# Kernel tuning notes

Hardware: AMD Instinct MI355X
Metric: run time of the kernel (lower is better)

The kernel has to match this reference:

```python
import jax, jax.numpy as jnp
import numpy as np


def gcn_conv(x, edge_index, W, b):
    # PyG GCNConv with normalize=True: add self-loops, symmetric D^-1/2 A D^-1/2,
    # transform then aggregate messages source->target, then add bias.
    N = x.shape[0]
    row, col = edge_index[0], edge_index[1]  # row: source, col: target
    loop = jnp.arange(N, dtype=edge_index.dtype)
    row = jnp.concatenate([row, loop])
    col = jnp.concatenate([col, loop])
    ones = jnp.ones(row.shape[0], dtype=x.dtype)
    deg = jax.ops.segment_sum(ones, col, num_segments=N)
    dinv = jnp.where(deg > 0, jax.lax.rsqrt(deg), 0.0)
    norm = dinv[row] * dinv[col]            # [E+N]
    h = x @ W                                # [N, d_out] transform first (cheaper aggregation)
    msgs = h[row] * norm[:, None]            # gather + scale
    out = jax.ops.segment_sum(msgs, col, num_segments=N)  # scatter-add to targets
    return out + b


def setup_inputs() -> dict:
    key = jax.random.key(0)
    k = jax.random.split(key, 6)
    N, D, H, C, E = 100000, 256, 32, 2, 3200000
    x = jax.random.normal(k[0], (N, D), dtype=jnp.float32)
    edge_index = jax.random.randint(k[1], (2, E), 0, N, dtype=jnp.int64)
    # glorot-style init for GCN weights
    W1 = jax.random.normal(k[2], (D, H), dtype=jnp.float32) * np.sqrt(2.0 / (D + H))
    b1 = jnp.zeros((H,), dtype=jnp.float32)
    W2 = jax.random.normal(k[3], (H, C), dtype=jnp.float32) * np.sqrt(2.0 / (H + C))
    b2 = jnp.zeros((C,), dtype=jnp.float32)
    return {"x": x, "edge_index": edge_index, "W1": W1, "b1": b1, "W2": W2, "b2": b2}


def reference(x, edge_index, W1, b1, W2, b2):
    # CRD: GCNConv -> relu -> dropout(p=0.5, eval mode -> identity)
    h = jax.nn.relu(gcn_conv(x, edge_index, W1, b1))
    # CLS: GCNConv -> log_softmax over classes
    logits = gcn_conv(h, edge_index, W2, b2)
    return jax.nn.log_softmax(logits, axis=1)
```

## Files before the change

### kernel.cpp

```cpp
#include <hip/hip_runtime.h>
#include <hip/hip_fp16.h>
#include <math.h>

#define DIV_UP(a,b) (((a)+(b)-1)/(b))

typedef _Float16 f16x8 __attribute__((ext_vector_type(8)));
typedef float    f32x4 __attribute__((ext_vector_type(4)));

#define SHIFT 9
#define TPB   (1 << SHIFT)
#define LMASK (TPB - 1)
#define CHUNK 4096

__global__ __launch_bounds__(256) void k_init(int* __restrict__ gcur, int cap,
                                              int* __restrict__ offsets, int N, int E) {
    const int t = threadIdx.x;
    gcur[t] = t * cap;
    if (t == 0) offsets[N] = E;
}

__global__ __launch_bounds__(256) void k_binA(const int* __restrict__ row,
                                              const int* __restrict__ col,
                                              int* __restrict__ gcur,
                                              unsigned* __restrict__ binned, int E) {
    __shared__ int hist[256], loff[256], gbase[256], lcur[256];
    __shared__ unsigned staged[CHUNK];
    __shared__ unsigned char binOf[CHUNK];
    const int t = threadIdx.x;
    const int base = blockIdx.x * CHUNK;
    const int n = min(CHUNK, E - base);

    hist[t] = 0;
    __syncthreads();

    unsigned pk[CHUNK / 256];
    int bn[CHUNK / 256];
#pragma unroll
    for (int k = 0; k < CHUNK / 256; ++k) {
        int i = base + t + k * 256;
        if (i < E) {
            int c = col[i], r = row[i];
            bn[k] = c >> SHIFT;
            pk[k] = ((unsigned)r << SHIFT) | (unsigned)(c & LMASK);
            atomicAdd(&hist[bn[k]], 1);
        } else bn[k] = -1;
    }
    __syncthreads();

    int v = hist[t];
    loff[t] = v;
    __syncthreads();
#pragma unroll
    for (int off = 1; off < 256; off <<= 1) {
        int y = (t >= off) ? loff[t - off] : 0;
        __syncthreads();
        loff[t] += y;
        __syncthreads();
    }
    int excl = loff[t] - v;
    gbase[t] = v ? atomicAdd(&gcur[t], v) : 0;
    lcur[t]  = excl;
    __syncthreads();
    loff[t] = excl;
    __syncthreads();

#pragma unroll
    for (int k = 0; k < CHUNK / 256; ++k) {
        if (bn[k] >= 0) {
            int p = atomicAdd(&lcur[bn[k]], 1);
            staged[p] = pk[k];
            binOf[p] = (unsigned char)bn[k];
        }
    }
    __syncthreads();

    for (int i = t; i < n; i += 256) {
        int b = binOf[i];
        binned[gbase[b] + (i - loff[b])] = staged[i];
    }
}

__global__ __launch_bounds__(256) void k_bscan2(const int* __restrict__ gcur, int cap,
                                                int* __restrict__ srcBase, int E) {
    __shared__ int sh[256];
    const int t = threadIdx.x;
    int cnt = gcur[t] - t * cap;
    sh[t] = cnt;
    __syncthreads();
#pragma unroll
    for (int off = 1; off < 256; off <<= 1) {
        int y = (t >= off) ? sh[t - off] : 0;
        __syncthreads();
        sh[t] += y;
        __syncthreads();
    }
    srcBase[t] = sh[t] - cnt;
    if (t == 255) srcBase[256] = E;
}

__global__ __launch_bounds__(512) void k_csr(const unsigned* __restrict__ binned,
                                             const int* __restrict__ gcur, int cap,
                                             const int* __restrict__ srcBase,
                                             int* __restrict__ offsets,
                                             float* __restrict__ dinv,
                                             int* __restrict__ srcs, int N) {
    __shared__ int h[TPB];
    __shared__ int cur[TPB];
    const int t = threadIdx.x, b = blockIdx.x;
    const int beg = b * cap, end = gcur[b];
    const int obase = srcBase[b];

    h[t] = 0;
    __syncthreads();
    for (int i = beg + t; i < end; i += 512)
        atomicAdd(&h[binned[i] & LMASK], 1);
    __syncthreads();

    int cnt = h[t];
#pragma unroll
    for (int off = 1; off < 512; off <<= 1) {
        int y = (t >= off) ? h[t - off] : 0;
        __syncthreads();
        h[t] += y;
        __syncthreads();
    }
    int excl = h[t] - cnt;
    int g = (b << SHIFT) + t;
    int pos0 = obase + excl;
    if (g < N) {
        offsets[g] = pos0;
        dinv[g] = rsqrtf((float)(1 + cnt));
    }
    cur[t] = pos0;
    __syncthreads();

    for (int i = beg + t; i < end; i += 512) {
        unsigned v = binned[i];
        int pos = atomicAdd(&cur[v & LMASK], 1);
        srcs[pos] = (int)(v >> SHIFT);
    }
}

__global__ __launch_bounds__(256) void k_gemm1(const float* __restrict__ x,
                                               const float* __restrict__ W,
                                               const float* __restrict__ dinv,
                                               __half* __restrict__ h1w, int N) {
    __shared__ float Wl[8192];
    const int t = threadIdx.x;

    const float4* W4 = (const float4*)W;
    float4* Wl4 = (float4*)Wl;
#pragma unroll
    for (int i = 0; i < 8; ++i) Wl4[t + 256 * i] = W4[t + 256 * i];
    __syncthreads();

    const int lane = t & 63;
    const int wv   = t >> 6;
    const int m    = lane & 15;
    const int q    = lane >> 4;

    f16x8 bf[8][2];
#pragma unroll
    for (int kc = 0; kc < 8; ++kc)
#pragma unroll
        for (int ct = 0; ct < 2; ++ct)
#pragma unroll
            for (int j = 0; j < 8; ++j)
                bf[kc][ct][j] = (_Float16)Wl[(kc * 32 + q * 8 + j) * 32 + ct * 16 + m];

    const int rowA   = blockIdx.x * 64 + wv * 16 + m;
    const int rclamp = min(rowA, N - 1);
    const float* xr  = x + (long long)rclamp * 256 + q * 8;

    f32x4 c0 = {0.f, 0.f, 0.f, 0.f}, c1 = {0.f, 0.f, 0.f, 0.f};
#pragma unroll
    for (int kc = 0; kc < 8; ++kc) {
        float4 v0 = *(const float4*)(xr + kc * 32);
        float4 v1 = *(const float4*)(xr + kc * 32 + 4);
        f16x8 a;
        a[0] = (_Float16)v0.x; a[1] = (_Float16)v0.y;
        a[2] = (_Float16)v0.z; a[3] = (_Float16)v0.w;
        a[4] = (_Float16)v1.x; a[5] = (_Float16)v1.y;
        a[6] = (_Float16)v1.z; a[7] = (_Float16)v1.w;
        c0 = __builtin_amdgcn_mfma_f32_16x16x32_f16(a, bf[kc][0], c0, 0, 0, 0);
        c1 = __builtin_amdgcn_mfma_f32_16x16x32_f16(a, bf[kc][1], c1, 0, 0, 0);
    }

    const int orow = blockIdx.x * 64 + wv * 16 + q * 4;
#pragma unroll
    for (int r = 0; r < 4; ++r) {
        int gr = orow + r;
        if (gr < N) {
            float di = dinv[gr];
            h1w[gr * 32 + m]      = __float2half(di * c0[r]);
            h1w[gr * 32 + 16 + m] = __float2half(di * c1[r]);
        }
    }
}

__global__ void k_agg1(const int* __restrict__ offsets, const int* __restrict__ srcs,
                       const float* __restrict__ dinv, const __half* __restrict__ h1w,
                       const float* __restrict__ b1, const float* __restrict__ W2,
                       __half2* __restrict__ tw, int N) {
    long long g = (long long)blockIdx.x * blockDim.x + threadIdx.x;
    int node = (int)(g >> 5), f = (int)(g & 31);
    if (node >= N) return;
    const int sub = f >> 2, q = f & 3;
    const int beg = offsets[node], end = offsets[node + 1];
    const uint4* h4 = (const uint4*)h1w;

    float a0 = 0.f, a1 = 0.f, a2 = 0.f, a3 = 0.f;
    float a4 = 0.f, a5 = 0.f, a6 = 0.f, a7 = 0.f;

    for (int j = beg; j < end; j += 8) {
        int e = j + sub;
        int ee = min(e, end - 1);
        int s = srcs[ee];
        float msk = (e < end) ? 1.f : 0.f;
        uint4 rv = h4[s * 4 + q];
        __half2 p; float2 u;
        p = *(__half2*)&rv.x; u = __half22float2(p); a0 = fmaf(u.x, msk, a0); a1 = fmaf(u.y, msk, a1);
        p = *(__half2*)&rv.y; u = __half22float2(p); a2 = fmaf(u.x, msk, a2); a3 = fmaf(u.y, msk, a3);
        p = *(__half2*)&rv.z; u = __half22float2(p); a4 = fmaf(u.x, msk, a4); a5 = fmaf(u.y, msk, a5);
        p = *(__half2*)&rv.w; u = __half22float2(p); a6 = fmaf(u.x, msk, a6); a7 = fmaf(u.y, msk, a7);
    }
#pragma unroll
    for (int s = 4; s < 32; s <<= 1) {
        a0 += __shfl_xor(a0, s, 32); a1 += __shfl_xor(a1, s, 32);
        a2 += __shfl_xor(a2, s, 32); a3 += __shfl_xor(a3, s, 32);
        a4 += __shfl_xor(a4, s, 32); a5 += __shfl_xor(a5, s, 32);
        a6 += __shfl_xor(a6, s, 32); a7 += __shfl_xor(a7, s, 32);
    }
    if (sub == 0) {
        float di = dinv[node];
        uint4 rv = h4[node * 4 + q];
        float sf[8];
        {
            __half2 p; float2 u;
            p = *(__half2*)&rv.x; u = __half22float2(p); sf[0] = u.x; sf[1] = u.y;
            p = *(__half2*)&rv.y; u = __half22float2(p); sf[2] = u.x; sf[3] = u.y;
            p = *(__half2*)&rv.z; u = __half22float2(p); sf[4] = u.x; sf[5] = u.y;
            p = *(__half2*)&rv.w; u = __half22float2(p); sf[6] = u.x; sf[7] = u.y;
        }
        float av[8] = {a0, a1, a2, a3, a4, a5, a6, a7};
        float t0 = 0.f, t1 = 0.f;
#pragma unroll
        for (int k = 0; k < 8; ++k) {
            int feat = q * 8 + k;
            float hv = fmaf(di, av[k] + sf[k], b1[feat]);
            hv = fmaxf(hv, 0.f);
            t0 = fmaf(hv, W2[feat * 2 + 0], t0);
            t1 = fmaf(hv, W2[feat * 2 + 1], t1);
        }
        t0 += __shfl_xor(t0, 1, 32); t0 += __shfl_xor(t0, 2, 32);
        t1 += __shfl_xor(t1, 1, 32); t1 += __shfl_xor(t1, 2, 32);
        if (q == 0) tw[node] = __floats2half2_rn(di * t0, di * t1);
    }
}

__global__ void k_agg2(const int* __restrict__ offsets, const int* __restrict__ srcs,
                       const float* __restrict__ dinv, const __half2* __restrict__ tw,
                       const float* __restrict__ b2, float* __restrict__ out, int N) {
    long long g = (long long)blockIdx.x * blockDim.x + threadIdx.x;
    int node = (int)(g >> 4), f = (int)(g & 15);
    if (node >= N) return;
    int beg = offsets[node], end = offsets[node + 1];
    float a0 = 0.f, a1 = 0.f;
    for (int j = beg + f; j < end; j += 16) {
        int s = srcs[j];
        float2 u = __half22float2(tw[s]);
        a0 += u.x;
        a1 += u.y;
    }
#pragma unroll
    for (int s = 8; s; s >>= 1) {
        a0 += __shfl_xor(a0, s, 64);
        a1 += __shfl_xor(a1, s, 64);
    }
    if (f == 0) {
        float di = dinv[node];
        float2 u = __half22float2(tw[node]);
        float z0 = di * (a0 + u.x) + b2[0];
        float z1 = di * (a1 + u.y) + b2[1];
        float m = fmaxf(z0, z1);
        float lse = m + logf(expf(z0 - m) + expf(z1 - m));
        ((float2*)out)[node] = float2{z0 - lse, z1 - lse};
    }
}

extern "C" void kernel_launch(void* const* d_in, const int* in_sizes, int n_in,
                              void* d_out, int out_size, void* d_ws, size_t ws_size,
                              hipStream_t stream) {
    const float* x  = (const float*)d_in[0];
    const int*   ei = (const int*)d_in[1];
    const float* W1 = (const float*)d_in[2];
    const float* b1 = (const float*)d_in[3];
    const float* W2 = (const float*)d_in[4];
    const float* b2 = (const float*)d_in[5];

    const int H = in_sizes[3];
    const int D = in_sizes[2] / H;
    const int N = in_sizes[0] / D;
    const int E = in_sizes[1] / 2;
    (void)H; (void)n_in; (void)out_size; (void)ws_size;

    const int* row = ei;
    const int* col = ei + E;

    const int K_used = ((N - 1) >> SHIFT) + 1;
    const int cap    = (DIV_UP(E, K_used) * 5 / 4 + 255) & ~255;
    const int nchunk = DIV_UP(E, CHUNK);

    char* p = (char*)d_ws;
    auto alloc = [&](size_t bytes) { char* q = p; p += (bytes + 255) & ~(size_t)255; return q; };
    int*      offsets = (int*)     alloc((size_t)(N + 1) * 4);
    int*      gcur    = (int*)     alloc(256 * 4);
    int*      srcBase = (int*)     alloc(257 * 4);
    float*    dinv    = (float*)   alloc((size_t)N * 4);
    unsigned* binned  = (unsigned*)alloc((size_t)K_used * cap * 4);
    __half*   h1w     = (__half*)  alloc((size_t)N * 32 * 2);
    int*      srcs    = (int*)     alloc((size_t)E * 4);
    __half2*  tw      = (__half2*) alloc((size_t)N * 4);

    k_init  <<<1, 256, 0, stream>>>(gcur, cap, offsets, N, E);
    k_binA  <<<nchunk, 256, 0, stream>>>(row, col, gcur, binned, E);
    k_bscan2<<<1, 256, 0, stream>>>(gcur, cap, srcBase, E);
    k_csr   <<<K_used, 512, 0, stream>>>(binned, gcur, cap, srcBase, offsets, dinv, srcs, N);
    k_gemm1 <<<DIV_UP(N, 64), 256, 0, stream>>>(x, W1, dinv, h1w, N);
    k_agg1  <<<(int)DIV_UP((long long)N * 32, 256), 256, 0, stream>>>(offsets, srcs, dinv, h1w, b1, W2, tw, N);
    k_agg2  <<<(int)DIV_UP((long long)N * 16, 256), 256, 0, stream>>>(offsets, srcs, dinv, tw, b2, (float*)d_out, N);
}
```

Measured before the change: 303.3 us.

## Fuse GEMM with edge binning in one launch and fold bin scan into CSR

The dense x@W1 GEMM and the edge-binning pass now run as two block ranges of one launch, so the compute-heavy and memory-heavy work can overlap on the GPU. The separate bin-offset scan kernel is replaced by a per-block reduction inside the CSR kernel. The dinv row scaling moves from the GEMM epilogue into the CSR kernel, which rescales h1 in place. This cuts two launches and serialization, at the cost of an extra read-modify-write of h1, one more fp16 rounding step, and larger shared memory in the fused kernel.

```diff
diff --git a/kernel.cpp b/kernel.cpp
--- a/kernel.cpp
+++ b/kernel.cpp
@@ -19,99 +19,150 @@
     if (t == 0) offsets[N] = E;
 }
 
-__global__ __launch_bounds__(256) void k_binA(const int* __restrict__ row,
-                                              const int* __restrict__ col,
-                                              int* __restrict__ gcur,
-                                              unsigned* __restrict__ binned, int E) {
-    __shared__ int hist[256], loff[256], gbase[256], lcur[256];
-    __shared__ unsigned staged[CHUNK];
-    __shared__ unsigned char binOf[CHUNK];
+__global__ __launch_bounds__(256) void k_fat(const float* __restrict__ x,
+                                             const float* __restrict__ W,
+                                             __half* __restrict__ h1,
+                                             const int* __restrict__ row,
+                                             const int* __restrict__ col,
+                                             int* __restrict__ gcur,
+                                             unsigned* __restrict__ binned,
+                                             int E, int N, int gemmB) {
+    __shared__ __align__(16) char smem[32768];
     const int t = threadIdx.x;
-    const int base = blockIdx.x * CHUNK;
-    const int n = min(CHUNK, E - base);
-
-    hist[t] = 0;
-    __syncthreads();
-
-    unsigned pk[CHUNK / 256];
-    int bn[CHUNK / 256];
-#pragma unroll
-    for (int k = 0; k < CHUNK / 256; ++k) {
-        int i = base + t + k * 256;
-        if (i < E) {
-            int c = col[i], r = row[i];
-            bn[k] = c >> SHIFT;
-            pk[k] = ((unsigned)r << SHIFT) | (unsigned)(c & LMASK);
-            atomicAdd(&hist[bn[k]], 1);
-        } else bn[k] = -1;
-    }
-    __syncthreads();
-
-    int v = hist[t];
-    loff[t] = v;
-    __syncthreads();
-#pragma unroll
-    for (int off = 1; off < 256; off <<= 1) {
-        int y = (t >= off) ? loff[t - off] : 0;
-        __syncthreads();
-        loff[t] += y;
-        __syncthreads();
-    }
-    int excl = loff[t] - v;
-    gbase[t] = v ? atomicAdd(&gcur[t], v) : 0;
-    lcur[t]  = excl;
-    __syncthreads();
-    loff[t] = excl;
-    __syncthreads();
-
-#pragma unroll
-    for (int k = 0; k < CHUNK / 256; ++k) {
-        if (bn[k] >= 0) {
-            int p = atomicAdd(&lcur[bn[k]], 1);
-            staged[p] = pk[k];
-            binOf[p] = (unsigned char)bn[k];
-        }
-    }
-    __syncthreads();
-
-    for (int i = t; i < n; i += 256) {
-        int b = binOf[i];
-        binned[gbase[b] + (i - loff[b])] = staged[i];
-    }
-}
-
-__global__ __launch_bounds__(256) void k_bscan2(const int* __restrict__ gcur, int cap,
-                                                int* __restrict__ srcBase, int E) {
-    __shared__ int sh[256];
-    const int t = threadIdx.x;
-    int cnt = gcur[t] - t * cap;
-    sh[t] = cnt;
-    __syncthreads();
-#pragma unroll
-    for (int off = 1; off < 256; off <<= 1) {
-        int y = (t >= off) ? sh[t - off] : 0;
-        __syncthreads();
-        sh[t] += y;
-        __syncthreads();
-    }
-    srcBase[t] = sh[t] - cnt;
-    if (t == 255) srcBase[256] = E;
-}
-
-__global__ __launch_bounds__(512) void k_csr(const unsigned* __restrict__ binned,
-                                             const int* __restrict__ gcur, int cap,
-                                             const int* __restrict__ srcBase,
-                                             int* __restrict__ offsets,
-                                             float* __restrict__ dinv,
-                                             int* __restrict__ srcs, int N) {
+
+    if ((int)blockIdx.x < gemmB) {
+        float* Wl = (float*)smem;
+        const float4* W4 = (const float4*)W;
+        float4* Wl4 = (float4*)Wl;
+#pragma unroll
+        for (int i = 0; i < 8; ++i) Wl4[t + 256 * i] = W4[t + 256 * i];
+        __syncthreads();
+
+        const int lane = t & 63;
+        const int wv   = t >> 6;
+        const int m    = lane & 15;
+        const int q    = lane >> 4;
+
+        f16x8 bf[8][2];
+#pragma unroll
+        for (int kc = 0; kc < 8; ++kc)
+#pragma unroll
+            for (int ct = 0; ct < 2; ++ct)
+#pragma unroll
+                for (int j = 0; j < 8; ++j)
+                    bf[kc][ct][j] = (_Float16)Wl[(kc * 32 + q * 8 + j) * 32 + ct * 16 + m];
+
+        const int rowA   = blockIdx.x * 64 + wv * 16 + m;
+        const int rclamp = min(rowA, N - 1);
+        const float* xr  = x + (long long)rclamp * 256 + q * 8;
+
+        f32x4 c0 = {0.f, 0.f, 0.f, 0.f}, c1 = {0.f, 0.f, 0.f, 0.f};
+#pragma unroll
+        for (int kc = 0; kc < 8; ++kc) {
+            float4 v0 = *(const float4*)(xr + kc * 32);
+            float4 v1 = *(const float4*)(xr + kc * 32 + 4);
+            f16x8 a;
+            a[0] = (_Float16)v0.x; a[1] = (_Float16)v0.y;
+            a[2] = (_Float16)v0.z; a[3] = (_Float16)v0.w;
+            a[4] = (_Float16)v1.x; a[5] = (_Float16)v1.y;
+            a[6] = (_Float16)v1.z; a[7] = (_Float16)v1.w;
+            c0 = __builtin_amdgcn_mfma_f32_16x16x32_f16(a, bf[kc][0], c0, 0, 0, 0);
+            c1 = __builtin_amdgcn_mfma_f32_16x16x32_f16(a, bf[kc][1], c1, 0, 0, 0);
+        }
+
+        const int orow = blockIdx.x * 64 + wv * 16 + q * 4;
+#pragma unroll
+        for (int r = 0; r < 4; ++r) {
+            int gr = orow + r;
+            if (gr < N) {
+                h1[gr * 32 + m]      = __float2half(c0[r]);
+                h1[gr * 32 + 16 + m] = __float2half(c1[r]);
+            }
+        }
+    } else {
+        int* hist  = (int*)smem;
+        int* loff  = hist + 256;
+        int* gbase = loff + 256;
+        int* lcur  = gbase + 256;
+        unsigned* staged     = (unsigned*)(smem + 4096);
+        unsigned char* binOf = (unsigned char*)(smem + 4096 + 16384);
+
+        const int base = (blockIdx.x - gemmB) * CHUNK;
+        const int n = min(CHUNK, E - base);
+
+        hist[t] = 0;
+        __syncthreads();
+
+        unsigned pk[CHUNK / 256];
+        int bn[CHUNK / 256];
+#pragma unroll
+        for (int k = 0; k < CHUNK / 256; ++k) {
+            int i = base + t + k * 256;
+            if (i < E) {
+                int c = col[i], r = row[i];
+                bn[k] = c >> SHIFT;
+                pk[k] = ((unsigned)r << SHIFT) | (unsigned)(c & LMASK);
+                atomicAdd(&hist[bn[k]], 1);
+            } else bn[k] = -1;
+        }
+        __syncthreads();
+
+        int v = hist[t];
+        loff[t] = v;
+        __syncthreads();
+#pragma unroll
+        for (int off = 1; off < 256; off <<= 1) {
+            int y = (t >= off) ? loff[t - off] : 0;
+            __syncthreads();
+            loff[t] += y;
+            __syncthreads();
+        }
+        int excl = loff[t] - v;
+        gbase[t] = v ? atomicAdd(&gcur[t], v) : 0;
+        lcur[t]  = excl;
+        __syncthreads();
+        loff[t] = excl;
+        __syncthreads();
+
+#pragma unroll
+        for (int k = 0; k < CHUNK / 256; ++k) {
+            if (bn[k] >= 0) {
+                int p = atomicAdd(&lcur[bn[k]], 1);
+                staged[p] = pk[k];
+                binOf[p] = (unsigned char)bn[k];
+            }
+        }
+        __syncthreads();
+
+        for (int i = t; i < n; i += 256) {
+            int b = binOf[i];
+            binned[gbase[b] + (i - loff[b])] = staged[i];
+        }
+    }
+}
+
+__global__ __launch_bounds__(512) void k_csr2(const unsigned* __restrict__ binned,
+                                              const int* __restrict__ gcur, int cap,
+                                              int* __restrict__ offsets,
+                                              float* __restrict__ dinv,
+                                              int* __restrict__ srcs,
+                                              __half* __restrict__ h1, int N) {
     __shared__ int h[TPB];
     __shared__ int cur[TPB];
+    __shared__ int rbuf[512];
     const int t = threadIdx.x, b = blockIdx.x;
     const int beg = b * cap, end = gcur[b];
-    const int obase = srcBase[b];
-
+
+    rbuf[t] = (t < 256 && t < b) ? (gcur[t] - t * cap) : 0;
     h[t] = 0;
     __syncthreads();
+#pragma unroll
+    for (int off = 256; off > 0; off >>= 1) {
+        if (t < off) rbuf[t] += rbuf[t + off];
+        __syncthreads();
+    }
+    const int obase = rbuf[0];
+
     for (int i = beg + t; i < end; i += 512)
         atomicAdd(&h[binned[i] & LMASK], 1);
     __syncthreads();
@@ -127,9 +178,11 @@
     int excl = h[t] - cnt;
     int g = (b << SHIFT) + t;
     int pos0 = obase + excl;
+    float di = 0.f;
     if (g < N) {
         offsets[g] = pos0;
-        dinv[g] = rsqrtf((float)(1 + cnt));
+        di = rsqrtf((float)(1 + cnt));
+        dinv[g] = di;
     }
     cur[t] = pos0;
     __syncthreads();
@@ -139,61 +192,19 @@
         int pos = atomicAdd(&cur[v & LMASK], 1);
         srcs[pos] = (int)(v >> SHIFT);
     }
-}
-
-__global__ __launch_bounds__(256) void k_gemm1(const float* __restrict__ x,
-                                               const float* __restrict__ W,
-                                               const float* __restrict__ dinv,
-                                               __half* __restrict__ h1w, int N) {
-    __shared__ float Wl[8192];
-    const int t = threadIdx.x;
-
-    const float4* W4 = (const float4*)W;
-    float4* Wl4 = (float4*)Wl;
-#pragma unroll
-    for (int i = 0; i < 8; ++i) Wl4[t + 256 * i] = W4[t + 256 * i];
-    __syncthreads();
-
-    const int lane = t & 63;
-    const int wv   = t >> 6;
-    const int m    = lane & 15;
-    const int q    = lane >> 4;
-
-    f16x8 bf[8][2];
-#pragma unroll
-    for (int kc = 0; kc < 8; ++kc)
-#pragma unroll
-        for (int ct = 0; ct < 2; ++ct)
-#pragma unroll
-            for (int j = 0; j < 8; ++j)
-                bf[kc][ct][j] = (_Float16)Wl[(kc * 32 + q * 8 + j) * 32 + ct * 16 + m];
-
-    const int rowA   = blockIdx.x * 64 + wv * 16 + m;
-    const int rclamp = min(rowA, N - 1);
-    const float* xr  = x + (long long)rclamp * 256 + q * 8;
-
-    f32x4 c0 = {0.f, 0.f, 0.f, 0.f}, c1 = {0.f, 0.f, 0.f, 0.f};
-#pragma unroll
-    for (int kc = 0; kc < 8; ++kc) {
-        float4 v0 = *(const float4*)(xr + kc * 32);
-        float4 v1 = *(const float4*)(xr + kc * 32 + 4);
-        f16x8 a;
-        a[0] = (_Float16)v0.x; a[1] = (_Float16)v0.y;
-        a[2] = (_Float16)v0.z; a[3] = (_Float16)v0.w;
-        a[4] = (_Float16)v1.x; a[5] = (_Float16)v1.y;
-        a[6] = (_Float16)v1.z; a[7] = (_Float16)v1.w;
-        c0 = __builtin_amdgcn_mfma_f32_16x16x32_f16(a, bf[kc][0], c0, 0, 0, 0);
-        c1 = __builtin_amdgcn_mfma_f32_16x16x32_f16(a, bf[kc][1], c1, 0, 0, 0);
-    }
-
-    const int orow = blockIdx.x * 64 + wv * 16 + q * 4;
-#pragma unroll
-    for (int r = 0; r < 4; ++r) {
-        int gr = orow + r;
-        if (gr < N) {
-            float di = dinv[gr];
-            h1w[gr * 32 + m]      = __float2half(di * c0[r]);
-            h1w[gr * 32 + 16 + m] = __float2half(di * c1[r]);
+
+    if (g < N) {
+        uint4* hp4 = (uint4*)(h1 + (size_t)g * 32);
+#pragma unroll
+        for (int k4 = 0; k4 < 4; ++k4) {
+            uint4 v = hp4[k4];
+            __half2* ph = (__half2*)&v;
+#pragma unroll
+            for (int k2 = 0; k2 < 4; ++k2) {
+                float2 u = __half22float2(ph[k2]);
+                ph[k2] = __floats2half2_rn(u.x * di, u.y * di);
+            }
+            hp4[k4] = v;
         }
     }
 }
@@ -310,23 +321,21 @@
     const int K_used = ((N - 1) >> SHIFT) + 1;
     const int cap    = (DIV_UP(E, K_used) * 5 / 4 + 255) & ~255;
     const int nchunk = DIV_UP(E, CHUNK);
+    const int gemmB  = DIV_UP(N, 64);
 
     char* p = (char*)d_ws;
     auto alloc = [&](size_t bytes) { char* q = p; p += (bytes + 255) & ~(size_t)255; return q; };
     int*      offsets = (int*)     alloc((size_t)(N + 1) * 4);
     int*      gcur    = (int*)     alloc(256 * 4);
-    int*      srcBase = (int*)     alloc(257 * 4);
     float*    dinv    = (float*)   alloc((size_t)N * 4);
     unsigned* binned  = (unsigned*)alloc((size_t)K_used * cap * 4);
-    __half*   h1w     = (__half*)  alloc((size_t)N * 32 * 2);
+    __half*   h1      = (__half*)  alloc((size_t)N * 32 * 2);
     int*      srcs    = (int*)     alloc((size_t)E * 4);
     __half2*  tw      = (__half2*) alloc((size_t)N * 4);
 
-    k_init  <<<1, 256, 0, stream>>>(gcur, cap, offsets, N, E);
-    k_binA  <<<nchunk, 256, 0, stream>>>(row, col, gcur, binned, E);
-    k_bscan2<<<1, 256, 0, stream>>>(gcur, cap, srcBase, E);
-    k_csr   <<<K_used, 512, 0, stream>>>(binned, gcur, cap, srcBase, offsets, dinv, srcs, N);
-    k_gemm1 <<<DIV_UP(N, 64), 256, 0, stream>>>(x, W1, dinv, h1w, N);
-    k_agg1  <<<(int)DIV_UP((long long)N * 32, 256), 256, 0, stream>>>(offsets, srcs, dinv, h1w, b1, W2, tw, N);
-    k_agg2  <<<(int)DIV_UP((long long)N * 16, 256), 256, 0, stream>>>(offsets, srcs, dinv, tw, b2, (float*)d_out, N);
-}
+    k_init <<<1, 256, 0, stream>>>(gcur, cap, offsets, N, E);
+    k_fat  <<<gemmB + nchunk, 256, 0, stream>>>(x, W1, h1, row, col, gcur, binned, E, N, gemmB);
+    k_csr2 <<<K_used, 512, 0, stream>>>(binned, gcur, cap, offsets, dinv, srcs, h1, N);
+    k_agg1 <<<(int)DIV_UP((long long)N * 32, 256), 256, 0, stream>>>(offsets, srcs, dinv, h1, b1, W2, tw, N);
+    k_agg2 <<<(int)DIV_UP((long long)N * 16, 256), 256, 0, stream>>>(offsets, srcs, dinv, tw, b2, (float*)d_out, N);
+}
```

Measured after the change: 295.1 us. 2.7% less time.
